# Kernel optimization log

Measured on AMD Instinct MI355X. Metric: run time of the kernel, lower is better.

The kernel has to match this reference:

```python
import jax, jax.numpy as jnp
import numpy as np

B, S, HID = 2, 2048, 2048
NH, NKV, HD = 32, 8, 64
EPS = 1e-6
SCALE = HD ** -0.5


def rms_norm(x, w, eps=EPS):
    xf = x.astype(jnp.float32)
    var = jnp.mean(xf * xf, axis=-1, keepdims=True)
    return (w * (xf * jax.lax.rsqrt(var + eps))).astype(x.dtype)


def rotate_half(x):
    x1, x2 = jnp.split(x, 2, axis=-1)
    return jnp.concatenate((-x2, x1), axis=-1)


def setup_inputs() -> dict:
    key = jax.random.key(0)
    ks = jax.random.split(key, 8)
    hidden_states = jax.random.normal(ks[0], (B, S, HID), jnp.float32)
    # realistic RoPE tables
    inv_freq = 1.0 / (500000.0 ** (np.arange(0, HD, 2, dtype=np.float32) / HD))
    pos = np.arange(S, dtype=np.float32)
    freqs = np.outer(pos, inv_freq)                      # [S, HD/2]
    emb = np.concatenate([freqs, freqs], axis=-1)        # [S, HD]
    cos = jnp.broadcast_to(jnp.asarray(np.cos(emb)), (B, S, HD))
    sin = jnp.broadcast_to(jnp.asarray(np.sin(emb)), (B, S, HD))
    std = HID ** -0.5
    Wq = jax.random.normal(ks[1], (NH * HD, HID), jnp.float32) * std
    Wk = jax.random.normal(ks[2], (NKV * HD, HID), jnp.float32) * std
    Wv = jax.random.normal(ks[3], (NKV * HD, HID), jnp.float32) * std
    Wo = jax.random.normal(ks[4], (HID, NH * HD), jnp.float32) * std
    q_norm_w = jnp.ones((HD,), jnp.float32)
    k_norm_w = jnp.ones((HD,), jnp.float32)
    return {"hidden_states": hidden_states, "cos": cos, "sin": sin,
            "Wq": Wq, "Wk": Wk, "Wv": Wv, "Wo": Wo,
            "q_norm_w": q_norm_w, "k_norm_w": k_norm_w}


def reference(hidden_states, cos, sin, Wq, Wk, Wv, Wo, q_norm_w, k_norm_w):
    b, s, _ = hidden_states.shape
    # QKV projections (nn.Linear: x @ W.T)
    q = (hidden_states @ Wq.T).reshape(b, s, NH, HD).transpose(0, 2, 1, 3)   # [B,NH,S,D]
    k = (hidden_states @ Wk.T).reshape(b, s, NKV, HD).transpose(0, 2, 1, 3)  # [B,NKV,S,D]
    v = (hidden_states @ Wv.T).reshape(b, s, NKV, HD).transpose(0, 2, 1, 3)
    # per-head QK RMSNorm (use_head_qk_norm=True)
    q = rms_norm(q, q_norm_w)
    k = rms_norm(k, k_norm_w)
    # RoPE, cos/sin broadcast over heads (unsqueeze dim 1)
    c = cos[:, None, :, :]
    sn = sin[:, None, :, :]
    q = q * c + rotate_half(q) * sn
    k = k * c + rotate_half(k) * sn
    # GQA: expand kv heads to query heads
    groups = NH // NKV
    k = jnp.repeat(k, groups, axis=1)
    v = jnp.repeat(v, groups, axis=1)
    # eager SDPA, causal, softmax in fp32
    scores = jnp.einsum('bhqd,bhkd->bhqk', q, k) * SCALE
    causal = jnp.tril(jnp.ones((s, s), bool))
    scores = jnp.where(causal, scores, jnp.finfo(jnp.float32).min)
    probs = jax.nn.softmax(scores.astype(jnp.float32), axis=-1).astype(q.dtype)
    attn = jnp.einsum('bhqk,bhkd->bhqd', probs, v)       # [B,NH,S,D]
    attn = attn.transpose(0, 2, 1, 3).reshape(b, s, NH * HD)
    return attn @ Wo.T
```

## Files before the change

kernel.cpp:

```cpp
#include <hip/hip_runtime.h>
#include <hip/hip_bf16.h>
#include <stdint.h>

typedef __bf16 bf16;
typedef __bf16 bf16x4 __attribute__((ext_vector_type(4)));
typedef __bf16 bf16x8 __attribute__((ext_vector_type(8)));
typedef float floatx4 __attribute__((ext_vector_type(4)));
typedef float floatx8 __attribute__((ext_vector_type(8)));

#define MFMA16(A, B, C) __builtin_amdgcn_mfma_f32_16x16x32_bf16(A, B, C, 0, 0, 0)

constexpr int Sc = 2048, HIDc = 2048, NHc = 32, NKVc = 8, HDc = 64;
constexpr float kScale = 0.125f;
constexpr float kMax = 9.0f;

__device__ __forceinline__ void async16(const bf16* g, bf16* l) {
  __builtin_amdgcn_global_load_lds(
      (const __attribute__((address_space(1))) void*)g,
      (__attribute__((address_space(3))) void*)l, 16, 0, 0);
}

__global__ __launch_bounds__(256)
void cvt5(const float* __restrict__ s0, bf16* __restrict__ d0, int n0,
          const float* __restrict__ s1, bf16* __restrict__ d1, int n1,
          const float* __restrict__ s2, bf16* __restrict__ d2, int n2,
          const float* __restrict__ s3, bf16* __restrict__ d3, int n3,
          const float* __restrict__ s4, bf16* __restrict__ d4, int n4)
{
  const float* s; bf16* d; int n;
  switch (blockIdx.y) {
    case 0: s = s0; d = d0; n = n0; break;
    case 1: s = s1; d = d1; n = n1; break;
    case 2: s = s2; d = d2; n = n2; break;
    case 3: s = s3; d = d3; n = n3; break;
    default: s = s4; d = d4; n = n4; break;
  }
  const size_t stride = (size_t)gridDim.x * blockDim.x * 8;
  for (size_t i = ((size_t)blockIdx.x * blockDim.x + threadIdx.x) * 8;
       i < (size_t)n; i += stride) {
    floatx8 f = *(const floatx8*)(s + i);
    bf16x8 o;
#pragma unroll
    for (int j = 0; j < 8; ++j) o[j] = (bf16)f[j];
    *(bf16x8*)(d + i) = o;
  }
}

template<int BM, int BN, bool SWZ>
__device__ __forceinline__
void gemm8p_core(const bf16* __restrict__ A, const bf16* __restrict__ Bw,
                 int K, int m0, int n0, bf16* __restrict__ lds,
                 floatx4 (&acc)[BM / 32][4])
{
  constexpr int MR2  = BM / 64;
  constexpr int ALD  = BM / 128;
  constexpr int BLD  = BN / 128;
  constexpr int AH   = BM * 32;
  constexpr int BH   = BN * 32;
  constexpr int GATE = ALD + BLD;
  constexpr int RS   = SWZ ? 1024 : 512;
  constexpr int MHS  = SWZ ? BM * 16 : MR2 * 512;

  const int tid  = threadIdx.x;
  const int lane = tid & 63;
  const int w    = tid >> 6;
  const int r    = lane & 15;
  const int quad = lane >> 4;
  const int wm   = w >> 2;
  const int wn   = w & 3;
  const int NT   = K >> 6;

  const bf16* gA[ALD]; const bf16* gB[BLD];
#pragma unroll
  for (int i = 0; i < ALD; ++i) {
    const int ch = i * 512 + tid;
    if constexpr (SWZ) {
      const int lrow = ch >> 3, sl = (ch & 7) ^ (lrow & 7);
      gA[i] = A + (size_t)(m0 + (sl >> 2) * (BM / 2) + lrow) * K + (sl & 3) * 8;
    } else {
      gA[i] = A + (size_t)(m0 + (ch >> 2)) * K + (ch & 3) * 8;
    }
  }
#pragma unroll
  for (int i = 0; i < BLD; ++i) {
    const int ch = i * 512 + tid;
    if constexpr (SWZ) {
      const int lrow = ch >> 3, sl = (ch & 7) ^ (lrow & 7);
      gB[i] = Bw + (size_t)(n0 + (sl >> 2) * (BN / 2) + lrow) * K + (sl & 3) * 8;
    } else {
      gB[i] = Bw + (size_t)(n0 + (ch >> 2)) * K + (ch & 3) * 8;
    }
  }

  auto stA = [&](int kt, int s, int kk) {
    bf16* dst = lds + (s * 2 + kk) * AH + tid * 8;
#pragma unroll
    for (int i = 0; i < ALD; ++i)
      async16(gA[i] + kt * 64 + kk * 32, dst + i * 4096);
  };
  auto stB = [&](int kt, int s, int kk) {
    bf16* dst = lds + 4 * AH + (s * 2 + kk) * BH + tid * 8;
#pragma unroll
    for (int i = 0; i < BLD; ++i)
      async16(gB[i] + kt * 64 + kk * 32, dst + i * 4096);
  };

  int aoff, boff;
  if constexpr (SWZ) {
    aoff = r * 64 + (((wm << 2) + quad) ^ (r & 7)) * 8;
    boff = ((wn & 1) * 64 + r) * 64 + ((((wn >> 1) << 2) + quad) ^ (r & 7)) * 8;
  } else {
    aoff = (wm * (BM / 2) + r) * 32 + quad * 8;
    boff = (wn * 64 + r) * 32 + quad * 8;
  }

  bf16x8 a[MR2], b[4];

#define LDB(S, KK) do { const bf16* _p = lds + 4 * AH + ((S) * 2 + (KK)) * BH + boff; \
  _Pragma("unroll") for (int n2 = 0; n2 < 4; ++n2) b[n2] = *(const bf16x8*)(_p + n2 * RS); } while (0)
#define LDA(S, KK, MH) do { const bf16* _p = lds + ((S) * 2 + (KK)) * AH + aoff + (MH) * MHS; \
  _Pragma("unroll") for (int m2 = 0; m2 < MR2; ++m2) a[m2] = *(const bf16x8*)(_p + m2 * RS); } while (0)
#define MM(MH) do { __builtin_amdgcn_s_setprio(1); \
  _Pragma("unroll") for (int m2 = 0; m2 < MR2; ++m2) \
    _Pragma("unroll") for (int n2 = 0; n2 < 4; ++n2) \
      acc[(MH) * MR2 + m2][n2] = MFMA16(a[m2], b[n2], acc[(MH) * MR2 + m2][n2]); \
  __builtin_amdgcn_s_setprio(0); } while (0)
#define BAR() asm volatile("s_barrier" ::: "memory")
#define GATEW() do { if constexpr (GATE == 4) asm volatile("s_waitcnt vmcnt(4)" ::: "memory"); \
                     else                     asm volatile("s_waitcnt vmcnt(3)" ::: "memory"); } while (0)

  stA(0, 0, 0); stB(0, 0, 0); stA(0, 0, 1); stB(0, 0, 1);
  stA(1, 1, 0); stB(1, 1, 0);
  GATEW(); BAR();

  for (int t = 0; t < NT; ++t) {
    const int s = t & 1;
    LDB(s, 0); LDA(s, 0, 0);
    if (t + 1 < NT) stA(t + 1, s ^ 1, 1);
    BAR(); MM(0); BAR();
    LDA(s, 0, 1);
    if (t + 1 < NT) stB(t + 1, s ^ 1, 1);
    BAR(); MM(1); BAR();
    LDB(s, 1); LDA(s, 1, 0);
    if (t + 2 < NT) stA(t + 2, s, 0);
    BAR(); MM(0); BAR();
    LDA(s, 1, 1);
    if (t + 2 < NT) stB(t + 2, s, 0);
    BAR(); MM(1);
    GATEW(); BAR();
  }

#undef LDB
#undef LDA
#undef MM
#undef BAR
#undef GATEW
}

template<int MT, bool CF32>
__device__ __forceinline__
void epi_plain(const floatx4 (&acc)[MT][4], void* C, int N, int m0, int n0,
               int BMh, int wm, int wn, int r, int quad)
{
#pragma unroll
  for (int mt = 0; mt < MT; ++mt) {
#pragma unroll
    for (int nt = 0; nt < 4; ++nt) {
      const int row = m0 + wm * BMh + mt * 16 + quad * 4;
      const int col = n0 + wn * 64 + nt * 16 + r;
#pragma unroll
      for (int g = 0; g < 4; ++g) {
        const size_t ci = (size_t)(row + g) * N + col;
        if constexpr (CF32) ((float*)C)[ci] = acc[mt][nt][g];
        else                ((bf16*)C)[ci]  = (bf16)acc[mt][nt][g];
      }
    }
  }
}

template<int MT>
__device__ __forceinline__
void epi_k(const floatx4 (&acc)[MT][4], bf16* kws, const float* kw,
           const float* cp, const float* sp, int m0, int n0,
           int wm, int wn, int r, int quad)
{
  const int h = (n0 >> 6) + wn;
  const float w0 = kw[r], w1 = kw[16 + r], w2 = kw[32 + r], w3 = kw[48 + r];
#pragma unroll
  for (int mt = 0; mt < MT; ++mt) {
#pragma unroll
    for (int g = 0; g < 4; ++g) {
      const int row = m0 + wm * 128 + mt * 16 + quad * 4 + g;
      const float x0 = acc[mt][0][g], x1 = acc[mt][1][g];
      const float x2 = acc[mt][2][g], x3 = acc[mt][3][g];
      float ss = x0 * x0 + x1 * x1 + x2 * x2 + x3 * x3;
      ss += __shfl_xor(ss, 1); ss += __shfl_xor(ss, 2);
      ss += __shfl_xor(ss, 4); ss += __shfl_xor(ss, 8);
      const float rr = rsqrtf(ss * (1.0f / 64.0f) + 1e-6f);
      const float y0 = x0 * rr * w0, y1 = x1 * rr * w1;
      const float y2 = x2 * rr * w2, y3 = x3 * rr * w3;
      const float* cb = cp + (size_t)row * 64 + r;
      const float* sb = sp + (size_t)row * 64 + r;
      bf16* p = kws + (size_t)row * 512 + h * 64 + r;
      p[0]  = (bf16)(y0 * cb[0]  - y2 * sb[0]);
      p[16] = (bf16)(y1 * cb[16] - y3 * sb[16]);
      p[32] = (bf16)(y2 * cb[32] + y0 * sb[32]);
      p[48] = (bf16)(y3 * cb[48] + y1 * sb[48]);
    }
  }
}

template<int MT>
__device__ __forceinline__
void epi_v(const floatx4 (&acc)[MT][4], bf16* vt, int m0, int n0,
           int wm, int wn, int r, int quad)
{
  const int kvh = (n0 >> 6) + wn;
  const int b   = m0 >> 11;
  const int sb  = (m0 & 2047) + wm * 128 + quad * 4;
#pragma unroll
  for (int mt = 0; mt < MT; ++mt) {
#pragma unroll
    for (int nt = 0; nt < 4; ++nt) {
      const int d = nt * 16 + r;
      bf16x4 pk;
#pragma unroll
      for (int g = 0; g < 4; ++g) pk[g] = (bf16)acc[mt][nt][g];
      *(bf16x4*)(vt + ((size_t)((b * 8 + kvh) * 64 + d)) * Sc + sb + mt * 16) = pk;
    }
  }
}

__global__ __launch_bounds__(512, 2)
void qkv_gemm8(const bf16* __restrict__ hs,
               const bf16* __restrict__ Wq, const bf16* __restrict__ Wk,
               const bf16* __restrict__ Wv,
               bf16* __restrict__ q_ws, bf16* __restrict__ k_ws,
               bf16* __restrict__ vt_ws,
               const float* __restrict__ kw, const float* __restrict__ cp,
               const float* __restrict__ sp)
{
  __shared__ bf16 lds[2 * 2 * (256 + 256) * 32];
  const int wg  = blockIdx.x;
  const int swz = (wg & 7) * 24 + (wg >> 3);
  const int mi  = swz / 12, ni = swz % 12;
  const bf16* Bw; int n0;
  if (ni < 8)       { Bw = Wq; n0 = ni * 256; }
  else if (ni < 10) { Bw = Wk; n0 = (ni - 8) * 256; }
  else              { Bw = Wv; n0 = (ni - 10) * 256; }

  floatx4 acc[8][4] = {};
  gemm8p_core<256, 256, false>(hs, Bw, HIDc, mi * 256, n0, lds, acc);

  const int lane = threadIdx.x & 63, w = threadIdx.x >> 6;
  const int r = lane & 15, quad = lane >> 4;
  const int wm = w >> 2, wn = w & 3;
  if (ni < 8)
    epi_plain<8, false>(acc, q_ws, 2048, mi * 256, n0, 128, wm, wn, r, quad);
  else if (ni < 10)
    epi_k<8>(acc, k_ws, kw, cp, sp, mi * 256, n0, wm, wn, r, quad);
  else
    epi_v<8>(acc, vt_ws, mi * 256, n0, wm, wn, r, quad);
}

__global__ __launch_bounds__(512, 2)
void o_gemm8(const bf16* __restrict__ a_ws, const bf16* __restrict__ Wo,
             float* __restrict__ out)
{
  __shared__ bf16 lds[2 * 2 * (128 + 256) * 32];
  const int wg  = blockIdx.x;
  const int swz = (wg & 7) * 32 + (wg >> 3);
  const int mi  = swz >> 3, ni = swz & 7;

  floatx4 acc[4][4] = {};
  gemm8p_core<128, 256, true>(a_ws, Wo, NHc * HDc, mi * 128, ni * 256, lds, acc);

  const int lane = threadIdx.x & 63, w = threadIdx.x >> 6;
  const int r = lane & 15, quad = lane >> 4;
  const int wm = w >> 2, wn = w & 3;
  epi_plain<4, true>(acc, out, HIDc, mi * 128, ni * 256, 64, wm, wn, r, quad);
}

__global__ __launch_bounds__(256, 4)
void attn_fwd(const bf16* __restrict__ q, const bf16* __restrict__ k,
              const bf16* __restrict__ vt, bf16* __restrict__ o,
              const float* __restrict__ qw, const float* __restrict__ cp,
              const float* __restrict__ sp)
{
  __shared__ bf16 Ks[64 * 64];
  __shared__ bf16 Vs[64 * 64];
  __shared__ bf16 Ps[4][16 * 72];

  const int bi  = blockIdx.x;
  const int pa  = bi & 15;
  const int h   = (bi >> 4) & 31;
  const int b   = bi >> 9;
  const int kvh = h >> 2;
  const int tid = threadIdx.x, lane = tid & 63, w = tid >> 6;
  const int r = lane & 15, quad = lane >> 4;
  const int qt0 = 31 - pa, qt1 = pa;

  const floatx8 w0 = *(const floatx8*)(qw + quad * 8);
  const floatx8 w1 = *(const floatx8*)(qw + 32 + quad * 8);
  bf16x8 qf[2][2];
#pragma unroll
  for (int t = 0; t < 2; ++t) {
    const int qt = t == 0 ? qt0 : qt1;
    const int m = b * Sc + qt * 64 + w * 16 + r;
    const bf16* qp = q + (size_t)m * (NHc * HDc) + h * HDc + quad * 8;
    bf16x8 x0 = *(const bf16x8*)qp;
    bf16x8 x1 = *(const bf16x8*)(qp + 32);
    float ss = 0.f;
#pragma unroll
    for (int i = 0; i < 8; ++i)
      ss += (float)x0[i] * (float)x0[i] + (float)x1[i] * (float)x1[i];
    ss += __shfl_xor(ss, 16);
    ss += __shfl_xor(ss, 32);
    const float rq = rsqrtf(ss * (1.0f / 64.0f) + 1e-6f) * kScale;
    const floatx8 c0 = *(const floatx8*)(cp + (size_t)m * 64 + quad * 8);
    const floatx8 c1 = *(const floatx8*)(cp + (size_t)m * 64 + 32 + quad * 8);
    const floatx8 s0 = *(const floatx8*)(sp + (size_t)m * 64 + quad * 8);
    const floatx8 s1 = *(const floatx8*)(sp + (size_t)m * 64 + 32 + quad * 8);
    bf16x8 y0v, y1v;
#pragma unroll
    for (int i = 0; i < 8; ++i) {
      const float y0 = (float)x0[i] * rq * w0[i];
      const float y1 = (float)x1[i] * rq * w1[i];
      y0v[i] = (bf16)(y0 * c0[i] - y1 * s0[i]);
      y1v[i] = (bf16)(y1 * c1[i] + y0 * s1[i]);
    }
    qf[t][0] = y0v; qf[t][1] = y1v;
  }

  floatx4 accO[2][4] = {};
  float lsum[2][4] = {};

  const int kvr = tid >> 3;
  const int cx  = ((tid & 7) * 8) ^ (8 * (kvr & 7));
  const int xk  = 8 * (r & 7);

  const bf16* kp = k + (size_t)b * Sc * (NKVc * HDc) + kvh * HDc;
  const bf16* vp = vt + ((size_t)((b * NKVc + kvh) * 64)) * Sc;

  for (int j = 0; j <= qt0; ++j) {
    __syncthreads();
    {
      const bf16* kj = kp + (size_t)j * 64 * (NKVc * HDc);
      const bf16* vj = vp + j * 64;
      async16(kj + (size_t)kvr * (NKVc * HDc) + cx, Ks + tid * 8);
      async16(kj + (size_t)(kvr + 32) * (NKVc * HDc) + cx, Ks + (tid + 256) * 8);
      async16(vj + (size_t)kvr * Sc + cx, Vs + tid * 8);
      async16(vj + (size_t)(kvr + 32) * Sc + cx, Vs + (tid + 256) * 8);
    }
    __syncthreads();

#pragma unroll
    for (int t = 0; t < 2; ++t) {
      if (t == 1 && j > qt1) continue;
      const int qt = t == 0 ? qt0 : qt1;

      floatx4 sa[4];
#pragma unroll
      for (int nt = 0; nt < 4; ++nt) sa[nt] = floatx4{0.f, 0.f, 0.f, 0.f};
      __builtin_amdgcn_s_setprio(1);
#pragma unroll
      for (int nt = 0; nt < 4; ++nt) {
        const int kv = nt * 16 + r;
        const bf16x8 kb0 = *(const bf16x8*)(&Ks[kv * 64 + ((quad * 8) ^ xk)]);
        const bf16x8 kb1 = *(const bf16x8*)(&Ks[kv * 64 + ((quad * 8 + 32) ^ xk)]);
        sa[nt] = MFMA16(qf[t][0], kb0, sa[nt]);
        sa[nt] = MFMA16(qf[t][1], kb1, sa[nt]);
      }
      __builtin_amdgcn_s_setprio(0);

      if (j != qt) {
#pragma unroll
        for (int g = 0; g < 4; ++g)
#pragma unroll
          for (int nt = 0; nt < 4; ++nt) {
            const float p = __expf(sa[nt][g] - kMax);
            lsum[t][g] += p;
            Ps[w][(quad * 4 + g) * 72 + nt * 16 + r] = (bf16)p;
          }
      } else {
        const int maskbase = w * 16 + quad * 4;
#pragma unroll
        for (int g = 0; g < 4; ++g)
#pragma unroll
          for (int nt = 0; nt < 4; ++nt) {
            const float p = (nt * 16 + r <= maskbase + g)
                                ? __expf(sa[nt][g] - kMax) : 0.f;
            lsum[t][g] += p;
            Ps[w][(quad * 4 + g) * 72 + nt * 16 + r] = (bf16)p;
          }
      }

      const bf16x8 pa0 = *(const bf16x8*)(&Ps[w][r * 72 + quad * 8]);
      const bf16x8 pa1 = *(const bf16x8*)(&Ps[w][r * 72 + 32 + quad * 8]);
      __builtin_amdgcn_s_setprio(1);
#pragma unroll
      for (int dt = 0; dt < 4; ++dt) {
        const int d = dt * 16 + r;
        const bf16x8 vb0 = *(const bf16x8*)(&Vs[d * 64 + ((quad * 8) ^ xk)]);
        const bf16x8 vb1 = *(const bf16x8*)(&Vs[d * 64 + ((quad * 8 + 32) ^ xk)]);
        accO[t][dt] = MFMA16(pa0, vb0, accO[t][dt]);
        accO[t][dt] = MFMA16(pa1, vb1, accO[t][dt]);
      }
      __builtin_amdgcn_s_setprio(0);
    }
  }

#pragma unroll
  for (int t = 0; t < 2; ++t) {
    const int qt = t == 0 ? qt0 : qt1;
#pragma unroll
    for (int reg = 0; reg < 4; ++reg) {
      float l = lsum[t][reg];
#pragma unroll
      for (int off = 1; off < 16; off <<= 1) l += __shfl_xor(l, off);
      const float inv = 1.0f / l;
      const size_t row = (size_t)(b * Sc + qt * 64 + w * 16 + quad * 4 + reg);
#pragma unroll
      for (int dt = 0; dt < 4; ++dt)
        o[row * (NHc * HDc) + h * HDc + dt * 16 + r] = (bf16)(accO[t][dt][reg] * inv);
    }
  }
}

extern "C" void kernel_launch(void* const* d_in, const int* in_sizes, int n_in,
                              void* d_out, int out_size, void* d_ws, size_t ws_size,
                              hipStream_t stream)
{
  const float* hs = (const float*)d_in[0];
  const float* cp = (const float*)d_in[1];
  const float* sp = (const float*)d_in[2];
  const float* Wq = (const float*)d_in[3];
  const float* Wk = (const float*)d_in[4];
  const float* Wv = (const float*)d_in[5];
  const float* Wo = (const float*)d_in[6];
  const float* qw = (const float*)d_in[7];
  const float* kw = (const float*)d_in[8];
  float* out = (float*)d_out;

  char* ws = (char*)d_ws;
  bf16* q_ws  = (bf16*)ws;
  bf16* k_ws  = (bf16*)(ws + (16u << 20));
  bf16* vt_ws = (bf16*)(ws + (24u << 20));
  bf16* hs_b  = (bf16*)(ws + (28u << 20));
  bf16* Wq_b  = (bf16*)(ws + (44u << 20));
  bf16* Wk_b  = (bf16*)(ws + (52u << 20));
  bf16* Wv_b  = (bf16*)(ws + (54u << 20));
  bf16* Wo_b  = (bf16*)(ws + (56u << 20));
  bf16* a_ws  = q_ws;

  dim3 blk(256);
  cvt5<<<dim3(256, 5), blk, 0, stream>>>(
      hs, hs_b, 4096 * 2048, Wq, Wq_b, 2048 * 2048, Wk, Wk_b, 512 * 2048,
      Wv, Wv_b, 512 * 2048, Wo, Wo_b, 2048 * 2048);
  qkv_gemm8<<<dim3(192), dim3(512), 0, stream>>>(hs_b, Wq_b, Wk_b, Wv_b,
                                                 q_ws, k_ws, vt_ws, kw, cp, sp);
  attn_fwd<<<dim3(1024), blk, 0, stream>>>(q_ws, k_ws, vt_ws, a_ws, qw, cp, sp);
  o_gemm8<<<dim3(256), dim3(512), 0, stream>>>(a_ws, Wo_b, out);
}
```

Measured before the change: 296.6 us.

## Merge GEMM sub-phases into two per k-tile and enable LDS swizzle for QKV

The 8-wave GEMM main loop drops from four barrier-separated MFMA phases per k-tile to two. Both M-halves of A fragments are now loaded into a doubled register array before one larger MFMA block, and the A and B async stages are issued together. This halves the barrier count per iteration but raises VGPR pressure and changes how LDS reads, global loads and MFMA overlap. The QKV GEMM also switches to the swizzled LDS layout to cut bank conflicts.

New measurement: 294.0 us. About the same (-0.9%).

```diff
diff --git a/kernel.cpp b/kernel.cpp
--- a/kernel.cpp
+++ b/kernel.cpp
@@ -114,16 +114,17 @@
     boff = (wn * 64 + r) * 32 + quad * 8;
   }
 
-  bf16x8 a[MR2], b[4];
+  bf16x8 a[2 * MR2], b[4];
 
 #define LDB(S, KK) do { const bf16* _p = lds + 4 * AH + ((S) * 2 + (KK)) * BH + boff; \
   _Pragma("unroll") for (int n2 = 0; n2 < 4; ++n2) b[n2] = *(const bf16x8*)(_p + n2 * RS); } while (0)
 #define LDA(S, KK, MH) do { const bf16* _p = lds + ((S) * 2 + (KK)) * AH + aoff + (MH) * MHS; \
-  _Pragma("unroll") for (int m2 = 0; m2 < MR2; ++m2) a[m2] = *(const bf16x8*)(_p + m2 * RS); } while (0)
-#define MM(MH) do { __builtin_amdgcn_s_setprio(1); \
-  _Pragma("unroll") for (int m2 = 0; m2 < MR2; ++m2) \
-    _Pragma("unroll") for (int n2 = 0; n2 < 4; ++n2) \
-      acc[(MH) * MR2 + m2][n2] = MFMA16(a[m2], b[n2], acc[(MH) * MR2 + m2][n2]); \
+  _Pragma("unroll") for (int m2 = 0; m2 < MR2; ++m2) a[(MH) * MR2 + m2] = *(const bf16x8*)(_p + m2 * RS); } while (0)
+#define MM2() do { __builtin_amdgcn_s_setprio(1); \
+  _Pragma("unroll") for (int mh = 0; mh < 2; ++mh) \
+    _Pragma("unroll") for (int m2 = 0; m2 < MR2; ++m2) \
+      _Pragma("unroll") for (int n2 = 0; n2 < 4; ++n2) \
+        acc[mh * MR2 + m2][n2] = MFMA16(a[mh * MR2 + m2], b[n2], acc[mh * MR2 + m2][n2]); \
   __builtin_amdgcn_s_setprio(0); } while (0)
 #define BAR() asm volatile("s_barrier" ::: "memory")
 #define GATEW() do { if constexpr (GATE == 4) asm volatile("s_waitcnt vmcnt(4)" ::: "memory"); \
@@ -135,24 +136,18 @@
 
   for (int t = 0; t < NT; ++t) {
     const int s = t & 1;
-    LDB(s, 0); LDA(s, 0, 0);
-    if (t + 1 < NT) stA(t + 1, s ^ 1, 1);
-    BAR(); MM(0); BAR();
-    LDA(s, 0, 1);
-    if (t + 1 < NT) stB(t + 1, s ^ 1, 1);
-    BAR(); MM(1); BAR();
-    LDB(s, 1); LDA(s, 1, 0);
-    if (t + 2 < NT) stA(t + 2, s, 0);
-    BAR(); MM(0); BAR();
-    LDA(s, 1, 1);
-    if (t + 2 < NT) stB(t + 2, s, 0);
-    BAR(); MM(1);
+    LDB(s, 0); LDA(s, 0, 0); LDA(s, 0, 1);
+    if (t + 1 < NT) { stA(t + 1, s ^ 1, 1); stB(t + 1, s ^ 1, 1); }
+    BAR(); MM2(); BAR();
+    LDB(s, 1); LDA(s, 1, 0); LDA(s, 1, 1);
+    if (t + 2 < NT) { stA(t + 2, s, 0); stB(t + 2, s, 0); }
+    BAR(); MM2();
     GATEW(); BAR();
   }
 
 #undef LDB
 #undef LDA
-#undef MM
+#undef MM2
 #undef BAR
 #undef GATEW
 }
@@ -250,7 +245,7 @@
   else              { Bw = Wv; n0 = (ni - 10) * 256; }
 
   floatx4 acc[8][4] = {};
-  gemm8p_core<256, 256, false>(hs, Bw, HIDc, mi * 256, n0, lds, acc);
+  gemm8p_core<256, 256, true>(hs, Bw, HIDc, mi * 256, n0, lds, acc);
 
   const int lane = threadIdx.x & 63, w = threadIdx.x >> 6;
   const int r = lane & 15, quad = lane >> 4;
```
